# Kernel optimization log

Hardware: AMD Instinct MI355X
Metric: run time of the kernel (lower is better)

The kernel has to match this reference:

```python
import jax, jax.numpy as jnp
import numpy as np

N_NODES = 16384
N_EDGES = 131072
N_GRAPHS = 16
U_SZ, U_RED = 4096, 256
EDGE_H, EDGE_OUT = 1024, 512
NODE_H = 512
NODE_IN = 9  # 4 + 5, hard-coded in OGRENet
EDGE_IN = 1


def _lin_init(k, fan_in, fan_out):
    k1, k2 = jax.random.split(k)
    bound = 1.0 / np.sqrt(fan_in)
    W = jax.random.uniform(k1, (fan_in, fan_out), jnp.float32, -bound, bound)
    b = jax.random.uniform(k2, (fan_out,), jnp.float32, -bound, bound)
    return W, b


def setup_inputs() -> dict:
    key = jax.random.key(0)
    ks = jax.random.split(key, 16)
    inp = {
        "x": jax.random.normal(ks[0], (N_NODES, NODE_IN), jnp.float32),
        "edge_attr": jax.random.normal(ks[1], (N_EDGES, EDGE_IN), jnp.float32),
        "u": jax.random.normal(ks[2], (N_GRAPHS, U_SZ), jnp.float32),
        "edge_index": jax.random.randint(ks[3], (2, N_EDGES), 0, N_NODES, jnp.int64 if jax.config.jax_enable_x64 else jnp.int32).astype(jnp.int32),
        "batch": jnp.sort(jax.random.randint(ks[4], (N_NODES,), 0, N_GRAPHS)).astype(jnp.int32),
    }
    # global dim reduction 4096 -> 256
    inp["w_dr"], inp["b_dr"] = _lin_init(ks[5], U_SZ, U_RED)
    # edge MLP: in = 1 + 2*9 + 256 = 275
    e_in = EDGE_IN + 2 * NODE_IN + U_RED
    inp["e_w0"], inp["e_b0"] = _lin_init(ks[6], e_in, EDGE_H)
    inp["e_w1"], inp["e_b1"] = _lin_init(ks[7], EDGE_H, EDGE_H)
    inp["e_w2"], inp["e_b2"] = _lin_init(ks[8], EDGE_H, EDGE_H)
    inp["e_w3"], inp["e_b3"] = _lin_init(ks[9], EDGE_H, EDGE_H)
    inp["e_wf"], inp["e_bf"] = _lin_init(ks[10], EDGE_H, EDGE_OUT)
    # node mlp 1: in = 9 + 512 = 521
    inp["n1_w0"], inp["n1_b0"] = _lin_init(ks[11], NODE_IN + EDGE_OUT, NODE_H)
    inp["n1_w1"], inp["n1_b1"] = _lin_init(ks[12], NODE_H, NODE_H)
    # node mlp 2: in = 9 + 512 + 256 = 777, out = 1
    inp["n2_w0"], inp["n2_b0"] = _lin_init(ks[13], NODE_IN + NODE_H + U_RED, NODE_H)
    inp["n2_w1"], inp["n2_b1"] = _lin_init(ks[14], NODE_H, 1)
    return inp


def reference(x, edge_attr, u, edge_index, batch,
              w_dr, b_dr,
              e_w0, e_b0, e_w1, e_b1, e_w2, e_b2, e_w3, e_b3, e_wf, e_bf,
              n1_w0, n1_b0, n1_w1, n1_b1,
              n2_w0, n2_b0, n2_w1, n2_b1):
    relu = jax.nn.relu
    # select_dim_reduction
    u_r = u @ w_dr + b_dr  # [G, 256]
    row, col = edge_index[0], edge_index[1]
    # EdgeModel: cat([src, dest, edge_attr, u[batch[row]]])
    e_in = jnp.concatenate([x[row], x[col], edge_attr, u_r[batch[row]]], axis=1)
    h = relu(e_in @ e_w0 + e_b0)
    h = relu(h @ e_w1 + e_b1)
    h = relu(h @ e_w2 + e_b2)
    h = relu(h @ e_w3 + e_b3)
    e = h @ e_wf + e_bf  # [E, 512]
    # NodeModel: mlp1 on cat([x[col], edge_attr_new]) then scatter_mean by row
    n_in = jnp.concatenate([x[col], e], axis=1)
    h = relu(n_in @ n1_w0 + n1_b0)
    h = relu(h @ n1_w1 + n1_b1)  # [E, 512]
    agg = jax.ops.segment_sum(h, row, num_segments=N_NODES)
    cnt = jax.ops.segment_sum(jnp.ones((h.shape[0],), h.dtype), row, num_segments=N_NODES)
    agg = agg / jnp.maximum(cnt, 1.0)[:, None]  # scatter_mean (zeros stay zero)
    o = jnp.concatenate([x, agg, u_r[batch]], axis=1)
    o = relu(o @ n2_w0 + n2_b0) @ n2_w1 + n2_b1  # [N, 1]
    return jnp.squeeze(o, axis=-1)
```

## Files before the change

kernel.cpp:

```cpp
#include <hip/hip_runtime.h>
#include <type_traits>
#include <utility>
#include <cstdint>

typedef unsigned short u16;
typedef __attribute__((ext_vector_type(4))) float f32x4;
typedef __attribute__((ext_vector_type(8))) short s16x8;
typedef __attribute__((ext_vector_type(8))) __bf16 b16x8;

template <typename T, typename = void> struct MfmaTakes : std::false_type {};
template <typename T>
struct MfmaTakes<T, std::void_t<decltype(__builtin_amdgcn_mfma_f32_16x16x32_bf16(
    std::declval<T>(), std::declval<T>(), std::declval<f32x4>(), 0, 0, 0))>>
    : std::true_type {};
using abvec = std::conditional_t<MfmaTakes<s16x8>::value, s16x8, b16x8>;
static_assert(sizeof(abvec) == 16, "frag must be 4 VGPRs");

template <typename T>
__device__ __forceinline__ f32x4 mfma_bf16(T a, T b, f32x4 c) {
  return __builtin_amdgcn_mfma_f32_16x16x32_bf16(a, b, c, 0, 0, 0);
}

__device__ __forceinline__ float b2f(u16 v) {
  union { unsigned u; float f; } x; x.u = ((unsigned)v) << 16; return x.f;
}
__device__ __forceinline__ u16 f2b(float f) {
  union { float f; unsigned u; } x; x.f = f;
  unsigned r = x.u + 0x7fffu + ((x.u >> 16) & 1u);
  return (u16)(r >> 16);
}

__device__ __forceinline__ void gld16(const void* g, void* l) {
  auto gp = reinterpret_cast<const __attribute__((address_space(1))) unsigned int*>(
      reinterpret_cast<uintptr_t>(g));
  auto lp = reinterpret_cast<__attribute__((address_space(3))) unsigned int*>(
      reinterpret_cast<uintptr_t>(l));
  __builtin_amdgcn_global_load_lds(gp, lp, 16, 0, 0);
}

#define NN 16384
#define NE 131072
#define NG 16

__global__ void detect_dtype(const u16* __restrict__ x, int* __restrict__ flag) {
  __shared__ int cnt;
  if (threadIdx.x == 0) cnt = 0;
  __syncthreads();
  int local = 0;
#pragma unroll
  for (int i = 0; i < 8; i++) {
    u16 h = x[threadIdx.x * 8 + i];
    int e = (h >> 7) & 0xFF;
    if (h == 0 || (e >= 110 && e <= 134)) local++;
  }
  atomicAdd(&cnt, local);
  __syncthreads();
  if (threadIdx.x == 0) *flag = (cnt >= 1700) ? 1 : 0;
}

struct CvtJob {
  const void* src[14];
  void* dst[14];
  int n[14];
};

__global__ __launch_bounds__(256) void cvt_all(CvtJob jb, const int* __restrict__ flag) {
  const int idx = blockIdx.x * 256 + threadIdx.x;
  const int f = *flag;
  int off = 0;
#pragma unroll
  for (int j = 0; j < 14; j++) {
    const int nn = jb.n[j];
    if (idx < off + nn) {
      const int i = idx - off;
      u16 v = f ? ((const u16*)jb.src[j])[i]
                : f2b(((const float*)jb.src[j])[i]);
      ((u16*)jb.dst[j])[i] = v;
      return;
    }
    off += nn;
  }
}

__global__ __launch_bounds__(256, 3) void gemm_bt(
    const u16* __restrict__ A, const u16* __restrict__ Bt,
    const u16* __restrict__ bias, u16* __restrict__ C,
    int M, int N, int K, int ldc, int relu)
{
  __shared__ alignas(16) u16 smem[24576];
  const int tid = threadIdx.x;
  const int wave = tid >> 6, lane = tid & 63;
  const int m0 = blockIdx.x * 128, n0 = blockIdx.y * 128;

  const int srow = lane >> 2;
  const int kslot = lane & 3;
  const int sswz = (srow >> 1) & 3;
  const u16* gA = A + (size_t)(m0 + wave * 32 + srow) * K + (kslot ^ sswz) * 8;
  const u16* gB = Bt + (size_t)(n0 + wave * 32 + srow) * K + (kslot ^ sswz) * 8;
  const int loff = (wave * 32 + srow) * 32 + kslot * 8;

  const int wm = (wave >> 1) * 64;
  const int wn = (wave & 1) * 64;
  const int fr = lane & 15;
  const int fks = ((lane >> 4) ^ ((fr >> 1) & 3)) * 8;

  f32x4 acc[4][4] = {};
  const int NT = K >> 5;

#define STAGE(t, s) do { \
    const int o_ = (t) * 32; \
    u16* S_ = smem + (s) * 8192; \
    gld16(gA + o_, S_ + loff); gld16(gA + 16 * (size_t)K + o_, S_ + loff + 512); \
    gld16(gB + o_, S_ + 4096 + loff); gld16(gB + 16 * (size_t)K + o_, S_ + 4096 + loff + 512); \
  } while (0)

  STAGE(0, 0);
  if (NT > 1) {
    STAGE(1, 1);
    __asm__ volatile("s_waitcnt vmcnt(4)" ::: "memory");
  } else {
    __asm__ volatile("s_waitcnt vmcnt(0)" ::: "memory");
  }
  __builtin_amdgcn_s_barrier();

  int sl = 0;
  for (int t = 0; t < NT; t++) {
    if (t + 2 < NT) {
      const int sw = (sl + 2 >= 3) ? sl - 1 : sl + 2;
      STAGE(t + 2, sw);
    }
    const u16* As = smem + sl * 8192;
    const u16* Bs = As + 4096;
    abvec af[4], bf[4];
#pragma unroll
    for (int i = 0; i < 4; i++)
      af[i] = *(const abvec*)&As[(wm + i * 16 + fr) * 32 + fks];
#pragma unroll
    for (int i = 0; i < 4; i++)
      bf[i] = *(const abvec*)&Bs[(wn + i * 16 + fr) * 32 + fks];
    __builtin_amdgcn_s_setprio(1);
#pragma unroll
    for (int mi = 0; mi < 4; mi++)
#pragma unroll
      for (int ni = 0; ni < 4; ni++)
        acc[mi][ni] = mfma_bf16(af[mi], bf[ni], acc[mi][ni]);
    __builtin_amdgcn_s_setprio(0);
    if (t + 2 < NT) __asm__ volatile("s_waitcnt vmcnt(4)" ::: "memory");
    else            __asm__ volatile("s_waitcnt vmcnt(0)" ::: "memory");
    __builtin_amdgcn_s_barrier();
    sl = (sl == 2) ? 0 : sl + 1;
  }
#undef STAGE

  const int crow0 = (lane >> 4) * 4;
  float bv[4];
#pragma unroll
  for (int ni = 0; ni < 4; ni++) bv[ni] = b2f(bias[n0 + wn + ni * 16 + fr]);

  u16* W = smem + wave * 4096;
#pragma unroll
  for (int mi = 0; mi < 4; mi++) {
#pragma unroll
    for (int ni = 0; ni < 4; ni++) {
      f32x4 v = acc[mi][ni];
      const int colx = ni * 16 + fr;
      const int cl = colx & 7, ch = colx >> 3;
#pragma unroll
      for (int r = 0; r < 4; r++) {
        const int rowx = mi * 16 + crow0 + r;
        float f = v[r] + bv[ni];
        if (relu) f = fmaxf(f, 0.0f);
        W[rowx * 64 + ((ch ^ (rowx & 7)) << 3) + cl] = f2b(f);
      }
    }
  }
  __asm__ volatile("s_waitcnt lgkmcnt(0)" ::: "memory");
#pragma unroll
  for (int p = 0; p < 8; p++) {
    const int rowx = p * 8 + (lane >> 3);
    const int pc = lane & 7;
    const int lc = pc ^ (rowx & 7);
    s16x8 val = *(const s16x8*)&W[rowx * 64 + pc * 8];
    *(s16x8*)&C[(size_t)(m0 + wm + rowx) * ldc + n0 + wn + lc * 8] = val;
  }
}

__global__ __launch_bounds__(1024) void gemm256b(
    const u16* __restrict__ A, const u16* __restrict__ Bt,
    const u16* __restrict__ bias, u16* __restrict__ C,
    int K, int ldc, int relu)
{
  __shared__ alignas(16) u16 smem[49152];
  const int tid = threadIdx.x;
  const int wave = tid >> 6, lane = tid & 63;
  const int wr = wave >> 2, wc = wave & 3;
  const int m0 = blockIdx.x << 8, n0 = blockIdx.y << 8;

  const int srow = tid >> 2;
  const int kslot = tid & 3;
  const int sswz = (srow >> 1) & 3;
  const u16* gA = A  + (size_t)(m0 + srow) * K + (kslot ^ sswz) * 8;
  const u16* gB = Bt + (size_t)(n0 + srow) * K + (kslot ^ sswz) * 8;
  const int loff = tid * 8;

  const int fr = lane & 15;
  const int fks = ((lane >> 4) ^ ((fr >> 1) & 3)) * 8;
  const int aob = (wr * 64 + fr) * 32 + fks;
  const int bob = (wc * 64 + fr) * 32 + fks;

  f32x4 acc[4][4] = {};
  const int NT = K >> 5;

#define STAGE2(t, s) do { \
    const int o_ = (t) * 32; \
    u16* S_ = smem + (s) * 16384; \
    gld16(gA + o_, S_ + loff); gld16(gB + o_, S_ + 8192 + loff); \
  } while (0)

  STAGE2(0, 0);
  if (NT > 1) {
    STAGE2(1, 1);
    __asm__ volatile("s_waitcnt vmcnt(2)" ::: "memory");
  } else {
    __asm__ volatile("s_waitcnt vmcnt(0)" ::: "memory");
  }
  __builtin_amdgcn_s_barrier();

  int sl = 0;
  for (int t = 0; t < NT; t++) {
    if (t + 2 < NT) {
      const int sw = (sl + 2 >= 3) ? sl - 1 : sl + 2;
      STAGE2(t + 2, sw);
    }
    const u16* As = smem + sl * 16384;
    const u16* Bs = As + 8192;
    abvec af[4], bf[4];
#pragma unroll
    for (int i = 0; i < 4; i++)
      af[i] = *(const abvec*)&As[aob + i * 512];
#pragma unroll
    for (int i = 0; i < 4; i++)
      bf[i] = *(const abvec*)&Bs[bob + i * 512];
    __builtin_amdgcn_s_setprio(1);
#pragma unroll
    for (int mi = 0; mi < 4; mi++)
#pragma unroll
      for (int ni = 0; ni < 4; ni++)
        acc[mi][ni] = mfma_bf16(af[mi], bf[ni], acc[mi][ni]);
    __builtin_amdgcn_s_setprio(0);
    if (t + 2 < NT) __asm__ volatile("s_waitcnt vmcnt(2)" ::: "memory");
    else            __asm__ volatile("s_waitcnt vmcnt(0)" ::: "memory");
    __builtin_amdgcn_s_barrier();
    sl = (sl == 2) ? 0 : sl + 1;
  }
#undef STAGE2

  const int crow0 = (lane >> 4) * 4;
  float bv[4];
#pragma unroll
  for (int ni = 0; ni < 4; ni++) bv[ni] = b2f(bias[n0 + wc * 64 + ni * 16 + fr]);
  u16* W = smem + wave * 2048;
#pragma unroll
  for (int h = 0; h < 2; h++) {
    if (h) __asm__ volatile("s_waitcnt lgkmcnt(0)" ::: "memory");
#pragma unroll
    for (int mi = 0; mi < 4; mi++) {
#pragma unroll
      for (int nh = 0; nh < 2; nh++) {
        const int ni = h * 2 + nh;
        f32x4 v = acc[mi][ni];
        const int colx = nh * 16 + fr;
        const int cl = colx & 7, ch = colx >> 3;
#pragma unroll
        for (int r = 0; r < 4; r++) {
          const int rowx = mi * 16 + crow0 + r;
          float f = v[r] + bv[ni];
          if (relu) f = fmaxf(f, 0.0f);
          W[rowx * 32 + ((ch ^ (rowx & 3)) << 3) + cl] = f2b(f);
        }
      }
    }
    __asm__ volatile("s_waitcnt lgkmcnt(0)" ::: "memory");
#pragma unroll
    for (int p = 0; p < 4; p++) {
      const int rowx = p * 16 + (lane >> 2);
      const int pc = lane & 3;
      const int lc = pc ^ (rowx & 3);
      s16x8 val = *(const s16x8*)&W[rowx * 32 + pc * 8];
      *(s16x8*)&C[(size_t)(m0 + wr * 64 + rowx) * ldc + n0 + wc * 64 + h * 32 + lc * 8] = val;
    }
  }
}

__global__ __launch_bounds__(256) void transpose_pad(
    const void* __restrict__ src, u16* __restrict__ dst, int K, int N, int Kp,
    int perm, const int* __restrict__ flag)
{
  __shared__ u16 tile[32][33];
  const int f = *flag;
  const u16* s16p = (const u16*)src;
  const float* sfp = (const float*)src;
  const int kb = blockIdx.x * 32, nb = blockIdx.y * 32;
  const int tx = threadIdx.x & 31, ty = threadIdx.x >> 5;
#pragma unroll
  for (int i = 0; i < 32; i += 8) {
    int k = kb + ty + i, n = nb + tx;
    u16 v = 0;
    if (k < K && n < N)
      v = f ? s16p[(size_t)k * N + n] : f2b(sfp[(size_t)k * N + n]);
    tile[ty + i][tx] = v;
  }
  __syncthreads();
#pragma unroll
  for (int i = 0; i < 32; i += 8) {
    int n = nb + ty + i, k = kb + tx;
    if (n < N && k < Kp) {
      int nk = perm ? (k < 9 ? 512 + k : (k < 521 ? k - 9 : k)) : k;
      dst[(size_t)n * Kp + nk] = tile[tx][ty + i];
    }
  }
}

__global__ __launch_bounds__(256) void dim_reduce2(
    const u16* __restrict__ u, const void* __restrict__ w,
    float* __restrict__ uacc, const int* __restrict__ flag)
{
  const int g = blockIdx.x, kt = blockIdx.y, j = threadIdx.x;
  const int f = *flag;
  __shared__ u16 us[512];
  us[j] = u[g * 4096 + kt * 512 + j];
  us[256 + j] = u[g * 4096 + kt * 512 + 256 + j];
  __syncthreads();
  float acc = 0.0f;
  if (f) {
    const u16* wp = (const u16*)w + (size_t)(kt * 512) * 256 + j;
#pragma unroll 8
    for (int k = 0; k < 512; k++) acc += b2f(us[k]) * b2f(wp[(size_t)k * 256]);
  } else {
    const float* wp = (const float*)w + (size_t)(kt * 512) * 256 + j;
#pragma unroll 8
    for (int k = 0; k < 512; k++) acc += b2f(us[k]) * wp[(size_t)k * 256];
  }
  atomicAdd(&uacc[g * 256 + j], acc);
}

__global__ __launch_bounds__(256) void finish_ur(
    const float* __restrict__ uacc, const u16* __restrict__ bdr,
    u16* __restrict__ ur)
{
  const int i = blockIdx.x * 256 + threadIdx.x;
  ur[i] = f2b(uacc[i] + b2f(bdr[i & 255]));
}

__global__ __launch_bounds__(256) void count_edges(
    const int* __restrict__ row, int* __restrict__ cnt)
{
  const int e = blockIdx.x * 256 + threadIdx.x;
  if (e < NE) atomicAdd(&cnt[row[e]], 1);
}

__global__ __launch_bounds__(256) void prefix_offs(
    const int* __restrict__ cnt, int* __restrict__ offs, int* __restrict__ cursor)
{
  __shared__ int part[256];
  __shared__ int base[256];
  const int t = threadIdx.x;
  int s = 0;
#pragma unroll
  for (int i = 0; i < 64; i++) s += cnt[t * 64 + i];
  part[t] = s;
  __syncthreads();
  if (t == 0) {
    int r = 0;
    for (int i = 0; i < 256; i++) { base[i] = r; r += part[i]; }
  }
  __syncthreads();
  int r = base[t];
#pragma unroll
  for (int i = 0; i < 64; i++) {
    const int n = t * 64 + i;
    offs[n] = r; cursor[n] = r; r += cnt[n];
  }
  if (t == 255) offs[16384] = r;
}

__global__ __launch_bounds__(256) void build_perm(
    const int* __restrict__ row, int* __restrict__ cursor, int* __restrict__ eperm)
{
  const int e = blockIdx.x * 256 + threadIdx.x;
  const int pos = atomicAdd(&cursor[row[e]], 1);
  eperm[pos] = e;
}

__global__ __launch_bounds__(256) void build_ein(
    const u16* __restrict__ x, const u16* __restrict__ ea,
    const u16* __restrict__ ur, const int* __restrict__ row,
    const int* __restrict__ col, const int* __restrict__ batch,
    const int* __restrict__ eperm, u16* __restrict__ out, int e0)
{
  const int idx = blockIdx.x * 256 + threadIdx.x;
  const int le = idx / 40, g = idx % 40;
  const int c0 = g * 8;
  const int e = eperm[e0 + le];
  const int r = row[e];
  alignas(16) u16 v[8];
  if (c0 >= 24 && c0 + 8 <= 275) {
    const u16* up = &ur[batch[r] * 256 + (c0 - 19)];
#pragma unroll
    for (int j = 0; j < 8; j++) v[j] = up[j];
  } else {
    const int cl = col[e];
    const int b = batch[r];
#pragma unroll
    for (int j = 0; j < 8; j++) {
      const int c = c0 + j;
      u16 t;
      if (c < 9)        t = x[r * 9 + c];
      else if (c < 18)  t = x[cl * 9 + (c - 9)];
      else if (c == 18) t = ea[e];
      else if (c < 275) t = ur[b * 256 + (c - 19)];
      else              t = 0;
      v[j] = t;
    }
  }
  *(s16x8*)&out[(size_t)le * 320 + c0] = *(const s16x8*)v;
}

__global__ __launch_bounds__(256) void fill_nin1_tail(
    const u16* __restrict__ x, const int* __restrict__ col,
    const int* __restrict__ eperm, u16* __restrict__ out, int e0)
{
  const int idx = blockIdx.x * 256 + threadIdx.x;
  const int le = idx >> 2, j8 = idx & 3;
  const int c0 = 512 + j8 * 8;
  const int cl = col[eperm[e0 + le]];
  alignas(16) u16 v[8];
#pragma unroll
  for (int j = 0; j < 8; j++) {
    const int c = c0 + j;
    v[j] = (c < 521) ? x[cl * 9 + (c - 512)] : (u16)0;
  }
  *(s16x8*)&out[(size_t)le * 544 + c0] = *(const s16x8*)v;
}

__global__ __launch_bounds__(256) void seg_reduce(
    const u16* __restrict__ h, const int* __restrict__ offs,
    float* __restrict__ agg, int e0, int echunk)
{
  const int wave = threadIdx.x >> 6, lane = threadIdx.x & 63;
  const int n = blockIdx.x * 4 + wave;
  int lo = offs[n], hi = offs[n + 1];
  const int first = (lo >= e0);
  lo = lo > e0 ? lo : e0;
  const int e1 = e0 + echunk;
  hi = hi < e1 ? hi : e1;
  if (lo >= hi) return;
  const int c0 = lane * 8;
  float acc[8] = {};
  for (int i = lo; i < hi; i++) {
    s16x8 v = *(const s16x8*)&h[(size_t)(i - e0) * 512 + c0];
#pragma unroll
    for (int j = 0; j < 8; j++) acc[j] += b2f((u16)v[j]);
  }
  float* ap = &agg[(size_t)n * 512 + c0];
  if (first) {
#pragma unroll
    for (int j = 0; j < 8; j++) ap[j] = acc[j];
  } else {
#pragma unroll
    for (int j = 0; j < 8; j++) ap[j] += acc[j];
  }
}

__global__ __launch_bounds__(256) void build_nin2(
    const u16* __restrict__ x, const float* __restrict__ agg,
    const int* __restrict__ cnt, const u16* __restrict__ ur,
    const int* __restrict__ batch, u16* __restrict__ out, int n0)
{
  const int idx = blockIdx.x * 256 + threadIdx.x;
  const int le = idx / 100, g = idx % 100;
  const int c0 = g * 8;
  const int n = n0 + le;
  alignas(16) u16 v[8];
  if (c0 < 512) {
    const int cn = cnt[n];
    if (cn == 0) {
#pragma unroll
      for (int j = 0; j < 8; j++) v[j] = 0;
    } else {
      const float den = (float)cn;
      const f32x4* ap = (const f32x4*)&agg[(size_t)n * 512 + c0];
      f32x4 a0 = ap[0], a1 = ap[1];
#pragma unroll
      for (int j = 0; j < 4; j++) { v[j] = f2b(a0[j] / den); v[4 + j] = f2b(a1[j] / den); }
    }
  } else {
    const int b = batch[n];
#pragma unroll
    for (int j = 0; j < 8; j++) {
      const int c = c0 + j;
      u16 t;
      if (c < 521)      t = x[n * 9 + (c - 512)];
      else if (c < 777) t = ur[b * 256 + (c - 521)];
      else              t = 0;
      v[j] = t;
    }
  }
  *(s16x8*)&out[(size_t)le * 800 + c0] = *(const s16x8*)v;
}

__global__ __launch_bounds__(256) void final_dot(
    const u16* __restrict__ h, const u16* __restrict__ w,
    const u16* __restrict__ b, void* __restrict__ out, int n0,
    const int* __restrict__ flag)
{
  const int wave = threadIdx.x >> 6, lane = threadIdx.x & 63;
  const int n = blockIdx.x * 4 + wave;
  const u16* hp = h + (size_t)n * 512 + lane * 8;
  const u16* wp = w + lane * 8;
  float s = 0.0f;
#pragma unroll
  for (int i = 0; i < 8; i++) s += b2f(hp[i]) * b2f(wp[i]);
#pragma unroll
  for (int off = 32; off > 0; off >>= 1) s += __shfl_down(s, off, 64);
  if (lane == 0) {
    float r = s + b2f(b[0]);
    if (*flag) ((u16*)out)[n0 + n] = f2b(r);
    else       ((float*)out)[n0 + n] = r;
  }
}

constexpr size_t OFF_FLAG = 0;
constexpr size_t OFF_XC   = 64;
constexpr size_t OFF_EAC  = OFF_XC   + 147456ull * 2;
constexpr size_t OFF_UC   = OFF_EAC  + 131072ull * 2;
constexpr size_t OFF_BDR  = OFF_UC   + 65536ull * 2;
constexpr size_t OFF_EB0  = OFF_BDR  + 256ull * 2;
constexpr size_t OFF_EB1  = OFF_EB0  + 1024ull * 2;
constexpr size_t OFF_EB2  = OFF_EB1  + 1024ull * 2;
constexpr size_t OFF_EB3  = OFF_EB2  + 1024ull * 2;
constexpr size_t OFF_EBF  = OFF_EB3  + 1024ull * 2;
constexpr size_t OFF_N1B0 = OFF_EBF  + 512ull * 2;
constexpr size_t OFF_N1B1 = OFF_N1B0 + 512ull * 2;
constexpr size_t OFF_N2B0 = OFF_N1B1 + 512ull * 2;
constexpr size_t OFF_N2W1 = OFF_N2B0 + 512ull * 2;
constexpr size_t OFF_N2B1 = OFF_N2W1 + 512ull * 2;
constexpr size_t OFF_OFFS = (OFF_N2B1 + 64 + 63) & ~63ull;
constexpr size_t OFF_CUR  = OFF_OFFS + 16388ull * 4;
constexpr size_t OFF_UACC = OFF_CUR  + 16384ull * 4;
static_assert(OFF_UACC + 4096 * 4 < (1ull << 20), "params+small fit in 1MB");

constexpr size_t OFF_W0T  = 1ull << 20;
constexpr size_t OFF_W1T  = OFF_W0T  + 1024ull * 320 * 2;
constexpr size_t OFF_W2T  = OFF_W1T  + 1024ull * 1024 * 2;
constexpr size_t OFF_W3T  = OFF_W2T  + 1024ull * 1024 * 2;
constexpr size_t OFF_WFT  = OFF_W3T  + 1024ull * 1024 * 2;
constexpr size_t OFF_N1W0 = OFF_WFT  + 512ull * 1024 * 2;
constexpr size_t OFF_N1W1 = OFF_N1W0 + 512ull * 544 * 2;
constexpr size_t OFF_N2W0 = OFF_N1W1 + 512ull * 512 * 2;
constexpr size_t OFF_UR   = OFF_N2W0 + 512ull * 800 * 2;
constexpr size_t OFF_CNT  = OFF_UR   + 16ull * 256 * 2;
constexpr size_t OFF_AGG  = OFF_CNT  + 16384ull * 4;
constexpr size_t OFF_BUF0 = OFF_AGG  + 16384ull * 512 * 4;

extern "C" void kernel_launch(void* const* d_in, const int* in_sizes, int n_in,
                              void* d_out, int out_size, void* d_ws, size_t ws_size,
                              hipStream_t stream) {
  const void* x_r  = d_in[0];
  const void* ea_r = d_in[1];
  const void* u_r  = d_in[2];
  const int*  ei    = (const int*)d_in[3];
  const int*  batch = (const int*)d_in[4];
  const void* w_dr = d_in[5];
  const void* b_dr = d_in[6];
  const void* e_w0 = d_in[7];  const void* e_b0 = d_in[8];
  const void* e_w1 = d_in[9];  const void* e_b1 = d_in[10];
  const void* e_w2 = d_in[11]; const void* e_b2 = d_in[12];
  const void* e_w3 = d_in[13]; const void* e_b3 = d_in[14];
  const void* e_wf = d_in[15]; const void* e_bf = d_in[16];
  const void* n1w0 = d_in[17]; const void* n1b0 = d_in[18];
  const void* n1w1 = d_in[19]; const void* n1b1 = d_in[20];
  const void* n2w0 = d_in[21]; const void* n2b0 = d_in[22];
  const void* n2w1 = d_in[23]; const void* n2b1 = d_in[24];

  const int* row = ei;
  const int* col = ei + NE;

  char* ws = (char*)d_ws;
  int*   FLAG = (int*)(ws + OFF_FLAG);
  u16*   XC   = (u16*)(ws + OFF_XC);
  u16*   EAC  = (u16*)(ws + OFF_EAC);
  u16*   UC   = (u16*)(ws + OFF_UC);
  u16*   BDRC = (u16*)(ws + OFF_BDR);
  u16*   EB0C = (u16*)(ws + OFF_EB0);
  u16*   EB1C = (u16*)(ws + OFF_EB1);
  u16*   EB2C = (u16*)(ws + OFF_EB2);
  u16*   EB3C = (u16*)(ws + OFF_EB3);
  u16*   EBFC = (u16*)(ws + OFF_EBF);
  u16*   N1B0C= (u16*)(ws + OFF_N1B0);
  u16*   N1B1C= (u16*)(ws + OFF_N1B1);
  u16*   N2B0C= (u16*)(ws + OFF_N2B0);
  u16*   N2W1C= (u16*)(ws + OFF_N2W1);
  u16*   N2B1C= (u16*)(ws + OFF_N2B1);
  int*   OFFS = (int*)(ws + OFF_OFFS);
  int*   CUR  = (int*)(ws + OFF_CUR);
  float* UACC = (float*)(ws + OFF_UACC);
  u16*   W0T  = (u16*)(ws + OFF_W0T);
  u16*   W1T  = (u16*)(ws + OFF_W1T);
  u16*   W2T  = (u16*)(ws + OFF_W2T);
  u16*   W3T  = (u16*)(ws + OFF_W3T);
  u16*   WFT  = (u16*)(ws + OFF_WFT);
  u16*   N1W0T= (u16*)(ws + OFF_N1W0);
  u16*   N1W1T= (u16*)(ws + OFF_N1W1);
  u16*   N2W0T= (u16*)(ws + OFF_N2W0);
  u16*   UR   = (u16*)(ws + OFF_UR);
  int*   CNT  = (int*)(ws + OFF_CNT);
  float* AGG  = (float*)(ws + OFF_AGG);
  (void)in_sizes; (void)n_in; (void)out_size;

  int echunk = 16384;
  while (echunk > 2048 &&
         OFF_BUF0 + (size_t)echunk * 4096 + (size_t)NE * 4 > ws_size) echunk >>= 1;
  u16* P    = (u16*)(ws + OFF_BUF0);
  u16* Q    = (u16*)(ws + OFF_BUF0 + (size_t)echunk * 2048);
  int* EPRM = (int*)(ws + OFF_BUF0 + (size_t)echunk * 4096);
  const int nchunks = NE / echunk;
  const int nodch = echunk < NN ? echunk : NN;
  const int nodchn = NN / nodch;

  detect_dtype<<<1, 256, 0, stream>>>((const u16*)x_r, FLAG);

  CvtJob jb;
  const void* srcs[14] = {x_r, ea_r, u_r, b_dr, e_b0, e_b1, e_b2, e_b3,
                          e_bf, n1b0, n1b1, n2b0, n2w1, n2b1};
  void* dsts[14] = {XC, EAC, UC, BDRC, EB0C, EB1C, EB2C, EB3C,
                    EBFC, N1B0C, N1B1C, N2B0C, N2W1C, N2B1C};
  const int ns[14] = {147456, 131072, 65536, 256, 1024, 1024, 1024, 1024,
                      512, 512, 512, 512, 512, 1};
  int tot = 0;
  for (int j = 0; j < 14; j++) { jb.src[j] = srcs[j]; jb.dst[j] = dsts[j]; jb.n[j] = ns[j]; tot += ns[j]; }
  cvt_all<<<(tot + 255) / 256, 256, 0, stream>>>(jb, FLAG);

  transpose_pad<<<dim3(10, 32), 256, 0, stream>>>(e_w0, W0T,  275, 1024, 320, 0, FLAG);
  transpose_pad<<<dim3(32, 32), 256, 0, stream>>>(e_w1, W1T, 1024, 1024, 1024, 0, FLAG);
  transpose_pad<<<dim3(32, 32), 256, 0, stream>>>(e_w2, W2T, 1024, 1024, 1024, 0, FLAG);
  transpose_pad<<<dim3(32, 32), 256, 0, stream>>>(e_w3, W3T, 1024, 1024, 1024, 0, FLAG);
  transpose_pad<<<dim3(32, 16), 256, 0, stream>>>(e_wf, WFT, 1024, 512, 1024, 0, FLAG);
  transpose_pad<<<dim3(17, 16), 256, 0, stream>>>(n1w0, N1W0T, 521, 512, 544, 1, FLAG);
  transpose_pad<<<dim3(16, 16), 256, 0, stream>>>(n1w1, N1W1T, 512, 512, 512, 0, FLAG);
  transpose_pad<<<dim3(25, 16), 256, 0, stream>>>(n2w0, N2W0T, 777, 512, 800, 1, FLAG);

  (void)hipMemsetAsync(UACC, 0, 4096ull * 4, stream);
  (void)hipMemsetAsync(CNT, 0, 16384ull * 4, stream);

  dim_reduce2<<<dim3(NG, 8), 256, 0, stream>>>(UC, w_dr, UACC, FLAG);
  finish_ur<<<16, 256, 0, stream>>>(UACC, BDRC, UR);

  count_edges<<<NE / 256, 256, 0, stream>>>(row, CNT);
  prefix_offs<<<1, 256, 0, stream>>>(CNT, OFFS, CUR);
  build_perm<<<NE / 256, 256, 0, stream>>>(row, CUR, EPRM);

  for (int c = 0; c < nchunks; c++) {
    const int e0 = c * echunk;
    build_ein<<<echunk * 40 / 256, 256, 0, stream>>>(XC, EAC, UR, row, col, batch, EPRM, P, e0);
    gemm256b<<<dim3(echunk / 256, 4), 1024, 0, stream>>>(P, W0T, EB0C, Q, 320, 1024, 1);
    gemm256b<<<dim3(echunk / 256, 4), 1024, 0, stream>>>(Q, W1T, EB1C, P, 1024, 1024, 1);
    gemm256b<<<dim3(echunk / 256, 4), 1024, 0, stream>>>(P, W2T, EB2C, Q, 1024, 1024, 1);
    gemm256b<<<dim3(echunk / 256, 4), 1024, 0, stream>>>(Q, W3T, EB3C, P, 1024, 1024, 1);
    gemm_bt<<<dim3(echunk / 128, 4), 256, 0, stream>>>(P, WFT, EBFC, Q, echunk, 512, 1024, 544, 0);
    fill_nin1_tail<<<echunk * 4 / 256, 256, 0, stream>>>(XC, col, EPRM, Q, e0);
    gemm_bt<<<dim3(echunk / 128, 4), 256, 0, stream>>>(Q, N1W0T, N1B0C, P, echunk, 512, 544, 512, 1);
    gemm_bt<<<dim3(echunk / 128, 4), 256, 0, stream>>>(P, N1W1T, N1B1C, Q, echunk, 512, 512, 512, 1);
    seg_reduce<<<NN / 4, 256, 0, stream>>>(Q, OFFS, AGG, e0, echunk);
  }

  for (int c = 0; c < nodchn; c++) {
    const int n0 = c * nodch;
    build_nin2<<<nodch * 100 / 256, 256, 0, stream>>>(XC, AGG, CNT, UR, batch, P, n0);
    gemm_bt<<<dim3(nodch / 128, 4), 256, 0, stream>>>(P, N2W0T, N2B0C, Q, nodch, 512, 800, 512, 1);
    final_dot<<<nodch / 4, 256, 0, stream>>>(Q, N2W1C, N2B1C, d_out, n0, FLAG);
  }
}
```

Before: 1.797 ms.

## Fold final edge linear layer into node MLP first layer weights

Because the final edge layer has no activation, its weight and bias are multiplied into the edge part of node-MLP1's first layer once in setup. This yields a fused 1056-wide weight and a combined bias. Per chunk, the 1024x512 edge-output GEMM disappears, and the h3 activations (padded to 1056 with x[col] in the tail) feed straight into one 1056->512 GEMM. The trade is precomputing the fused weights at bf16 precision, with a slightly different rounding order, and a wider K in the fused GEMM.

```diff
diff --git a/kernel.cpp b/kernel.cpp
--- a/kernel.cpp
+++ b/kernel.cpp
@@ -82,6 +82,15 @@
   }
 }
 
+__global__ __launch_bounds__(256) void cvt_plain(
+    const void* __restrict__ src, u16* __restrict__ dst, int n,
+    const int* __restrict__ flag)
+{
+  const int i = blockIdx.x * 256 + threadIdx.x;
+  if (i >= n) return;
+  dst[i] = *flag ? ((const u16*)src)[i] : f2b(((const float*)src)[i]);
+}
+
 __global__ __launch_bounds__(256, 3) void gemm_bt(
     const u16* __restrict__ A, const u16* __restrict__ Bt,
     const u16* __restrict__ bias, u16* __restrict__ C,
@@ -294,7 +303,7 @@
 
 __global__ __launch_bounds__(256) void transpose_pad(
     const void* __restrict__ src, u16* __restrict__ dst, int K, int N, int Kp,
-    int perm, const int* __restrict__ flag)
+    int perm, int k0, const int* __restrict__ flag)
 {
   __shared__ u16 tile[32][33];
   const int f = *flag;
@@ -307,7 +316,7 @@
     int k = kb + ty + i, n = nb + tx;
     u16 v = 0;
     if (k < K && n < N)
-      v = f ? s16p[(size_t)k * N + n] : f2b(sfp[(size_t)k * N + n]);
+      v = f ? s16p[(size_t)(k0 + k) * N + n] : f2b(sfp[(size_t)(k0 + k) * N + n]);
     tile[ty + i][tx] = v;
   }
   __syncthreads();
@@ -319,6 +328,25 @@
       dst[(size_t)n * Kp + nk] = tile[tx][ty + i];
     }
   }
+}
+
+__global__ __launch_bounds__(256) void fuse_tail(
+    const u16* __restrict__ n1w0t, u16* __restrict__ fused)
+{
+  const int idx = blockIdx.x * 256 + threadIdx.x;
+  const int p = idx >> 5, t = idx & 31;
+  fused[p * 1056 + 1024 + t] = n1w0t[p * 544 + 512 + t];
+}
+
+__global__ __launch_bounds__(256) void fuse_bias(
+    const u16* __restrict__ ebf, const u16* __restrict__ n1b0,
+    const u16* __restrict__ n1w0e, u16* __restrict__ fb)
+{
+  const int p = blockIdx.x * 256 + threadIdx.x;
+  float acc = b2f(n1b0[p]);
+#pragma unroll 8
+  for (int j = 0; j < 512; j++) acc += b2f(ebf[j]) * b2f(n1w0e[p * 512 + j]);
+  fb[p] = f2b(acc);
 }
 
 __global__ __launch_bounds__(256) void dim_reduce2(
@@ -426,21 +454,21 @@
   *(s16x8*)&out[(size_t)le * 320 + c0] = *(const s16x8*)v;
 }
 
-__global__ __launch_bounds__(256) void fill_nin1_tail(
+__global__ __launch_bounds__(256) void fill_h_tail(
     const u16* __restrict__ x, const int* __restrict__ col,
     const int* __restrict__ eperm, u16* __restrict__ out, int e0)
 {
   const int idx = blockIdx.x * 256 + threadIdx.x;
   const int le = idx >> 2, j8 = idx & 3;
-  const int c0 = 512 + j8 * 8;
+  const int c0 = 1024 + j8 * 8;
   const int cl = col[eperm[e0 + le]];
   alignas(16) u16 v[8];
 #pragma unroll
   for (int j = 0; j < 8; j++) {
     const int c = c0 + j;
-    v[j] = (c < 521) ? x[cl * 9 + (c - 512)] : (u16)0;
-  }
-  *(s16x8*)&out[(size_t)le * 544 + c0] = *(const s16x8*)v;
+    v[j] = (c < 1033) ? x[cl * 9 + (c - 1024)] : (u16)0;
+  }
+  *(s16x8*)&out[(size_t)le * 1056 + c0] = *(const s16x8*)v;
 }
 
 __global__ __launch_bounds__(256) void seg_reduce(
@@ -554,11 +582,15 @@
 constexpr size_t OFF_W1T  = OFF_W0T  + 1024ull * 320 * 2;
 constexpr size_t OFF_W2T  = OFF_W1T  + 1024ull * 1024 * 2;
 constexpr size_t OFF_W3T  = OFF_W2T  + 1024ull * 1024 * 2;
-constexpr size_t OFF_WFT  = OFF_W3T  + 1024ull * 1024 * 2;
-constexpr size_t OFF_N1W0 = OFF_WFT  + 512ull * 1024 * 2;
+constexpr size_t OFF_WFC  = OFF_W3T  + 1024ull * 1024 * 2;
+constexpr size_t OFF_N1W0 = OFF_WFC  + 1024ull * 512 * 2;
 constexpr size_t OFF_N1W1 = OFF_N1W0 + 512ull * 544 * 2;
 constexpr size_t OFF_N2W0 = OFF_N1W1 + 512ull * 512 * 2;
-constexpr size_t OFF_UR   = OFF_N2W0 + 512ull * 800 * 2;
+constexpr size_t OFF_N1WE = OFF_N2W0 + 512ull * 800 * 2;
+constexpr size_t OFF_FUSE = OFF_N1WE + 512ull * 512 * 2;
+constexpr size_t OFF_FB   = OFF_FUSE + 512ull * 1056 * 2;
+constexpr size_t OFF_ZB   = OFF_FB   + 512ull * 2;
+constexpr size_t OFF_UR   = OFF_ZB   + 1024ull * 2;
 constexpr size_t OFF_CNT  = OFF_UR   + 16ull * 256 * 2;
 constexpr size_t OFF_AGG  = OFF_CNT  + 16384ull * 4;
 constexpr size_t OFF_BUF0 = OFF_AGG  + 16384ull * 512 * 4;
@@ -609,10 +641,14 @@
   u16*   W1T  = (u16*)(ws + OFF_W1T);
   u16*   W2T  = (u16*)(ws + OFF_W2T);
   u16*   W3T  = (u16*)(ws + OFF_W3T);
-  u16*   WFT  = (u16*)(ws + OFF_WFT);
+  u16*   WFC  = (u16*)(ws + OFF_WFC);
   u16*   N1W0T= (u16*)(ws + OFF_N1W0);
   u16*   N1W1T= (u16*)(ws + OFF_N1W1);
   u16*   N2W0T= (u16*)(ws + OFF_N2W0);
+  u16*   N1WE = (u16*)(ws + OFF_N1WE);
+  u16*   FUSED= (u16*)(ws + OFF_FUSE);
+  u16*   FB   = (u16*)(ws + OFF_FB);
+  u16*   ZB   = (u16*)(ws + OFF_ZB);
   u16*   UR   = (u16*)(ws + OFF_UR);
   int*   CNT  = (int*)(ws + OFF_CNT);
   float* AGG  = (float*)(ws + OFF_AGG);
@@ -620,10 +656,10 @@
 
   int echunk = 16384;
   while (echunk > 2048 &&
-         OFF_BUF0 + (size_t)echunk * 4096 + (size_t)NE * 4 > ws_size) echunk >>= 1;
+         OFF_BUF0 + (size_t)echunk * 4224 + (size_t)NE * 4 > ws_size) echunk >>= 1;
   u16* P    = (u16*)(ws + OFF_BUF0);
-  u16* Q    = (u16*)(ws + OFF_BUF0 + (size_t)echunk * 2048);
-  int* EPRM = (int*)(ws + OFF_BUF0 + (size_t)echunk * 4096);
+  u16* Q    = (u16*)(ws + OFF_BUF0 + (size_t)echunk * 2112);
+  int* EPRM = (int*)(ws + OFF_BUF0 + (size_t)echunk * 4224);
   const int nchunks = NE / echunk;
   const int nodch = echunk < NN ? echunk : NN;
   const int nodchn = NN / nodch;
@@ -641,17 +677,23 @@
   for (int j = 0; j < 14; j++) { jb.src[j] = srcs[j]; jb.dst[j] = dsts[j]; jb.n[j] = ns[j]; tot += ns[j]; }
   cvt_all<<<(tot + 255) / 256, 256, 0, stream>>>(jb, FLAG);
 
-  transpose_pad<<<dim3(10, 32), 256, 0, stream>>>(e_w0, W0T,  275, 1024, 320, 0, FLAG);
-  transpose_pad<<<dim3(32, 32), 256, 0, stream>>>(e_w1, W1T, 1024, 1024, 1024, 0, FLAG);
-  transpose_pad<<<dim3(32, 32), 256, 0, stream>>>(e_w2, W2T, 1024, 1024, 1024, 0, FLAG);
-  transpose_pad<<<dim3(32, 32), 256, 0, stream>>>(e_w3, W3T, 1024, 1024, 1024, 0, FLAG);
-  transpose_pad<<<dim3(32, 16), 256, 0, stream>>>(e_wf, WFT, 1024, 512, 1024, 0, FLAG);
-  transpose_pad<<<dim3(17, 16), 256, 0, stream>>>(n1w0, N1W0T, 521, 512, 544, 1, FLAG);
-  transpose_pad<<<dim3(16, 16), 256, 0, stream>>>(n1w1, N1W1T, 512, 512, 512, 0, FLAG);
-  transpose_pad<<<dim3(25, 16), 256, 0, stream>>>(n2w0, N2W0T, 777, 512, 800, 1, FLAG);
+  transpose_pad<<<dim3(10, 32), 256, 0, stream>>>(e_w0, W0T,  275, 1024, 320, 0, 0, FLAG);
+  transpose_pad<<<dim3(32, 32), 256, 0, stream>>>(e_w1, W1T, 1024, 1024, 1024, 0, 0, FLAG);
+  transpose_pad<<<dim3(32, 32), 256, 0, stream>>>(e_w2, W2T, 1024, 1024, 1024, 0, 0, FLAG);
+  transpose_pad<<<dim3(32, 32), 256, 0, stream>>>(e_w3, W3T, 1024, 1024, 1024, 0, 0, FLAG);
+  transpose_pad<<<dim3(17, 16), 256, 0, stream>>>(n1w0, N1W0T, 521, 512, 544, 1, 0, FLAG);
+  transpose_pad<<<dim3(16, 16), 256, 0, stream>>>(n1w1, N1W1T, 512, 512, 512, 0, 0, FLAG);
+  transpose_pad<<<dim3(25, 16), 256, 0, stream>>>(n2w0, N2W0T, 777, 512, 800, 1, 0, FLAG);
+  transpose_pad<<<dim3(16, 16), 256, 0, stream>>>(n1w0, N1WE, 512, 512, 512, 0, 9, FLAG);
+  cvt_plain<<<2048, 256, 0, stream>>>(e_wf, WFC, 1024 * 512, FLAG);
 
   (void)hipMemsetAsync(UACC, 0, 4096ull * 4, stream);
   (void)hipMemsetAsync(CNT, 0, 16384ull * 4, stream);
+  (void)hipMemsetAsync(ZB, 0, 2048, stream);
+
+  gemm_bt<<<dim3(4, 8), 256, 0, stream>>>(N1WE, WFC, ZB, FUSED, 512, 1024, 512, 1056, 0);
+  fuse_tail<<<64, 256, 0, stream>>>(N1W0T, FUSED);
+  fuse_bias<<<2, 256, 0, stream>>>(EBFC, N1B0C, N1WE, FB);
 
   dim_reduce2<<<dim3(NG, 8), 256, 0, stream>>>(UC, w_dr, UACC, FLAG);
   finish_ur<<<16, 256, 0, stream>>>(UACC, BDRC, UR);
@@ -666,12 +708,11 @@
     gemm256b<<<dim3(echunk / 256, 4), 1024, 0, stream>>>(P, W0T, EB0C, Q, 320, 1024, 1);
     gemm256b<<<dim3(echunk / 256, 4), 1024, 0, stream>>>(Q, W1T, EB1C, P, 1024, 1024, 1);
     gemm256b<<<dim3(echunk / 256, 4), 1024, 0, stream>>>(P, W2T, EB2C, Q, 1024, 1024, 1);
-    gemm256b<<<dim3(echunk / 256, 4), 1024, 0, stream>>>(Q, W3T, EB3C, P, 1024, 1024, 1);
-    gemm_bt<<<dim3(echunk / 128, 4), 256, 0, stream>>>(P, WFT, EBFC, Q, echunk, 512, 1024, 544, 0);
-    fill_nin1_tail<<<echunk * 4 / 256, 256, 0, stream>>>(XC, col, EPRM, Q, e0);
-    gemm_bt<<<dim3(echunk / 128, 4), 256, 0, stream>>>(Q, N1W0T, N1B0C, P, echunk, 512, 544, 512, 1);
-    gemm_bt<<<dim3(echunk / 128, 4), 256, 0, stream>>>(P, N1W1T, N1B1C, Q, echunk, 512, 512, 512, 1);
-    seg_reduce<<<NN / 4, 256, 0, stream>>>(Q, OFFS, AGG, e0, echunk);
+    gemm256b<<<dim3(echunk / 256, 4), 1024, 0, stream>>>(Q, W3T, EB3C, P, 1024, 1056, 1);
+    fill_h_tail<<<echunk * 4 / 256, 256, 0, stream>>>(XC, col, EPRM, P, e0);
+    gemm_bt<<<dim3(echunk / 128, 4), 256, 0, stream>>>(P, FUSED, FB, Q, echunk, 512, 1056, 512, 1);
+    gemm_bt<<<dim3(echunk / 128, 4), 256, 0, stream>>>(Q, N1W1T, N1B1C, P, echunk, 512, 512, 512, 1);
+    seg_reduce<<<NN / 4, 256, 0, stream>>>(P, OFFS, AGG, e0, echunk);
   }
 
   for (int c = 0; c < nodchn; c++) {
```

Result: faster. 1.755 ms (-2.4%).
